# Performance work log

Hardware: AMD Instinct MI355X
Metric: run time of the kernel (lower is better)

## Reference

```python
import jax, jax.numpy as jnp
import numpy as np

B, T_SRC, T_TGT = 2048, 32, 32
D = 512            # d_model
D_SRC, D_TGT = 100, 80
L = 2              # n_layers


def setup_inputs() -> dict:
    key = jax.random.key(0)
    ks = jax.random.split(key, 16)
    s = 1.0 / float(np.sqrt(D))  # torch LSTM init scale
    u = lambda k, shape: jax.random.uniform(k, shape, jnp.float32, -s, s)
    return {
        "src": jax.random.randint(ks[0], (B, T_SRC), 0, D_SRC, dtype=jnp.int32),
        "tgt": jax.random.randint(ks[1], (B, T_TGT), 0, D_TGT, dtype=jnp.int32),
        "enc_emb": jax.random.normal(ks[2], (D_SRC, D), jnp.float32),
        "dec_emb": jax.random.normal(ks[3], (D_TGT, D), jnp.float32),
        "enc_Wih": u(ks[4], (L, 4 * D, D)),
        "enc_Whh": u(ks[5], (L, 4 * D, D)),
        "enc_bih": u(ks[6], (L, 4 * D)),
        "enc_bhh": u(ks[7], (L, 4 * D)),
        "dec_Wih": u(ks[8], (L, 4 * D, D)),
        "dec_Whh": u(ks[9], (L, 4 * D, D)),
        "dec_bih": u(ks[10], (L, 4 * D)),
        "dec_bhh": u(ks[11], (L, 4 * D)),
        "post_W": u(ks[12], (D_TGT, D)),
        "post_b": u(ks[13], (D_TGT,)),
    }


def lstm_cell(x, h, c, Wih, Whh, bih, bhh):
    # PyTorch gate order: i, f, g, o
    gates = x @ Wih.T + bih + h @ Whh.T + bhh  # [B, 4D]
    i, f, g, o = jnp.split(gates, 4, axis=-1)
    c_new = jax.nn.sigmoid(f) * c + jax.nn.sigmoid(i) * jnp.tanh(g)
    h_new = jax.nn.sigmoid(o) * jnp.tanh(c_new)
    return h_new, c_new


def reference(src, tgt, enc_emb, dec_emb, enc_Wih, enc_Whh, enc_bih, enc_bhh,
              dec_Wih, dec_Whh, dec_bih, dec_bhh, post_W, post_b):
    # Eval-mode forward: dropout = identity, teacher forcing disabled
    # (tf = random() < ratio AND self.training is False at inference).
    n_layers = enc_Wih.shape[0]
    Bb = src.shape[0]
    Dm = enc_emb.shape[1]

    # ---- encoder: multi-layer LSTM over src embeddings ----
    x = enc_emb[src].swapaxes(0, 1)  # [T_src, B, D]
    hs, cs = [], []
    z = jnp.zeros((Bb, Dm), x.dtype)
    for l in range(n_layers):
        def step(carry, xt, l=l):
            h, c = carry
            h, c = lstm_cell(xt, h, c, enc_Wih[l], enc_Whh[l], enc_bih[l], enc_bhh[l])
            return (h, c), h
        (hT, cT), x = jax.lax.scan(step, (z, z), x)
        hs.append(hT)
        cs.append(cT)
    h0 = jnp.stack(hs)  # [L, B, D]
    c0 = jnp.stack(cs)  # [L, B, D]

    prev0 = dec_emb[tgt[:, 0]]  # [B, D]

    def dec_step(carry, _):
        h, c, prev = carry
        x = prev
        new_h, new_c = [], []
        for l in range(n_layers):
            hl, cl = lstm_cell(x, h[l], c[l], dec_Wih[l], dec_Whh[l], dec_bih[l], dec_bhh[l])
            new_h.append(hl)
            new_c.append(cl)
            x = hl
        logits = x @ post_W.T + post_b          # [B, d_tgt]
        pred = jnp.argmax(logits, axis=-1)       # [B]
        prev = dec_emb[pred]                     # [B, D]
        return (jnp.stack(new_h), jnp.stack(new_c), prev), logits

    _, out = jax.lax.scan(dec_step, (h0, c0, prev0), None, length=tgt.shape[1])
    return out.swapaxes(0, 1)  # [B, T_tgt, d_tgt]
```

## Files before the change

### kernel.cpp

```cpp
#include <hip/hip_runtime.h>
#include <hip/hip_bf16.h>

#define B_  2048
#define T_  32
#define D_  512
#define G_  2048
#define VT_ 80
#define BD  (B_ * D_)
#define LWE ((size_t)G_ * D_)

typedef _Float16 half8 __attribute__((ext_vector_type(8)));
typedef _Float16 half4_t __attribute__((ext_vector_type(4)));
typedef float    f32x4 __attribute__((ext_vector_type(4)));

static __device__ __forceinline__ float sigm(float x) {
    return 1.0f / (1.0f + expf(-x));
}

typedef __attribute__((address_space(1))) unsigned int gas_u32;
typedef __attribute__((address_space(3))) unsigned int las_u32;
static __device__ __forceinline__ void glds16(const void* src, void* dst) {
    __builtin_amdgcn_global_load_lds(
        (gas_u32*)(unsigned long long)(size_t)src,
        (las_u32*)(unsigned int)(size_t)dst, 16, 0, 0);
}

#define WBX() do {                                        \
    asm volatile("s_waitcnt vmcnt(10)" ::: "memory");     \
    __builtin_amdgcn_s_barrier();                         \
    __builtin_amdgcn_sched_barrier(0);                    \
} while (0)

__global__ void zero_ws(int4* __restrict__ p, int n) {
    int i = blockIdx.x * blockDim.x + threadIdx.x;
    if (i < n) p[i] = int4{0, 0, 0, 0};
}
__global__ void init_pred(const int* __restrict__ tgt, int* __restrict__ pred) {
    int i = blockIdx.x * blockDim.x + threadIdx.x;
    if (i < B_) pred[i] = tgt[i * T_];
}

__global__ void split_weights(const float* __restrict__ s0, const float* __restrict__ s1,
                              const float* __restrict__ s2, const float* __restrict__ s3,
                              const float* __restrict__ s4, const float* __restrict__ s5,
                              _Float16* __restrict__ Wbase) {
    int g = blockIdx.x * blockDim.x + threadIdx.x;
    int mat = g >> 17;
    int rem = g & 131071;
    int np  = rem >> 6;
    int kq  = rem & 63;
    const float* src = (mat == 0) ? s0 : (mat == 1) ? s1 : (mat == 2) ? s2
                     : (mat == 3) ? s3 : (mat == 4) ? s4 : s5;
    int n = (np & 3) * D_ + (np >> 2);
    const float* sp = src + (size_t)n * D_ + kq * 8;
    float4 v0 = ((const float4*)sp)[0], v1 = ((const float4*)sp)[1];
    float x[8] = {v0.x, v0.y, v0.z, v0.w, v1.x, v1.y, v1.z, v1.w};
    _Float16 hi[8], lo[8];
    #pragma unroll
    for (int u = 0; u < 8; ++u) {
        hi[u] = (_Float16)x[u];
        lo[u] = (_Float16)(x[u] - (float)hi[u]);
    }
    int tile = (np >> 4) * 16 + (kq >> 2);
    int lane = (np & 15) | ((kq & 3) << 4);
    size_t e = (size_t)tile * 512 + (size_t)lane * 8;
    _Float16* Whi = Wbase + (size_t)mat * (2 * LWE);
    _Float16* Wlo = Whi + LWE;
    *(half8*)(Whi + e) = *(half8*)hi;
    *(half8*)(Wlo + e) = *(half8*)lo;
}

__global__ void split_postW(const float* __restrict__ pw,
                            _Float16* __restrict__ Ph, _Float16* __restrict__ Pl) {
    int g = blockIdx.x * blockDim.x + threadIdx.x;
    if (g >= VT_ * 64) return;
    int v = g >> 6, kq = g & 63;
    const float* sp = pw + (size_t)v * D_ + kq * 8;
    float4 v0 = ((const float4*)sp)[0], v1 = ((const float4*)sp)[1];
    float x[8] = {v0.x, v0.y, v0.z, v0.w, v1.x, v1.y, v1.z, v1.w};
    _Float16 hi[8], lo[8];
    #pragma unroll
    for (int u = 0; u < 8; ++u) {
        hi[u] = (_Float16)x[u];
        lo[u] = (_Float16)(x[u] - (float)hi[u]);
    }
    int tile = (v >> 4) * 16 + (kq >> 2);
    int lane = (v & 15) | ((kq & 3) << 4);
    size_t e = (size_t)tile * 512 + (size_t)lane * 8;
    *(half8*)(Ph + e) = *(half8*)hi;
    *(half8*)(Pl + e) = *(half8*)lo;
}

__global__ void perm_bias(const float* __restrict__ ebih, const float* __restrict__ ebhh,
                          const float* __restrict__ dbih, const float* __restrict__ dbhh,
                          float* __restrict__ biasP) {
    int i = blockIdx.x * blockDim.x + threadIdx.x;
    int cfg = i >> 11, np = i & 2047;
    int n = (np & 3) * D_ + (np >> 2);
    const float* bi = ((cfg < 2) ? ebih : dbih) + (cfg & 1) * G_;
    const float* bh = ((cfg < 2) ? ebhh : dbhh) + (cfg & 1) * G_;
    biasP[cfg * G_ + np] = bi[n] + bh[n];
}

__global__ __launch_bounds__(256) void compute_P(
    const float* __restrict__ enc_emb, const float* __restrict__ dec_emb,
    const float* __restrict__ encW0,   const float* __restrict__ decW0,
    float* __restrict__ P) {
    __shared__ float es[10][D_];
    __shared__ float part[4][64][10];
    int by = blockIdx.y;
    bool enc = (by < 10);
    int r0 = enc ? by * 10 : 100 + (by - 10) * 10;
    int s0 = enc ? by * 10 : (by - 10) * 10;
    const float* emb = enc ? enc_emb : dec_emb;
    const float* W   = enc ? encW0 : decW0;
    int tid = threadIdx.x;
    #pragma unroll
    for (int it = 0; it < 5; ++it) {
        int i4 = it * 256 + tid;
        int rr = i4 >> 7, cc = i4 & 127;
        ((float4*)es[rr])[cc] = ((const float4*)(emb + (size_t)(s0 + rr) * D_))[cc];
    }
    __syncthreads();
    int o   = tid & 63;
    int seg = tid >> 6;
    int np = blockIdx.x * 64 + o;
    int n = (np & 3) * D_ + (np >> 2);
    const float* wr = W + (size_t)n * D_ + seg * 128;
    float acc[10];
    #pragma unroll
    for (int rr = 0; rr < 10; ++rr) acc[rr] = 0.f;
    for (int k = 0; k < 128; k += 4) {
        float4 w4 = *(const float4*)(wr + k);
        int kb = seg * 128 + k;
        #pragma unroll
        for (int rr = 0; rr < 10; ++rr)
            acc[rr] += es[rr][kb] * w4.x + es[rr][kb+1] * w4.y
                     + es[rr][kb+2] * w4.z + es[rr][kb+3] * w4.w;
    }
    #pragma unroll
    for (int rr = 0; rr < 10; ++rr) part[seg][o][rr] = acc[rr];
    __syncthreads();
    for (int i = tid; i < 640; i += 256) {
        int o2 = i & 63, rr = i >> 6;
        P[(size_t)(r0 + rr) * G_ + blockIdx.x * 64 + o2] =
            (part[0][o2][rr] + part[1][o2][rr]) + (part[2][o2][rr] + part[3][o2][rr]);
    }
}

struct CellJob {
    const _Float16 *a0h, *a0l, *w0h, *w0l;
    int kclo0, kchi0;
    const _Float16 *a1h, *a1l, *w1h, *w1l;
    int kclo1, kchi1;
    const float *biasP;
    const float *P;
    const int  *idx;
    int idx_stride, emb_rows;
    float *c_io;
    _Float16 *hh_out, *hl_out;
};

__global__ __launch_bounds__(512, 2) void lstm_cell_mfma(CellJob J0, CellJob J1) {
    const CellJob J = (blockIdx.z == 0) ? J0 : J1;
    __shared__ __align__(128) char smem[65536];
    float (*gf)[68] = (float (*)[68])smem;

    const int tid  = threadIdx.x;
    const int w    = tid >> 6;
    const int lane = tid & 63;
    const int g    = w >> 2;
    const int mw   = w & 3;
    const int id   = blockIdx.x;
    const int xcd  = id & 7;
    const int rest = id >> 3;
    const int mt   = ((rest & 3) << 1) | (xcd >> 2);
    const int bx   = ((rest >> 2) << 2) | (xcd & 3);
    const int m0   = mt * 256;

    const _Float16* Ah = g ? J.a1h : J.a0h;
    const _Float16* Al = g ? J.a1l : J.a0l;
    const _Float16* Wh = g ? J.w1h : J.w0h;
    const _Float16* Wl = g ? J.w1l : J.w0l;
    const int kclo = g ? J.kclo1 : J.kclo0;
    const int kchi = g ? J.kchi1 : J.kchi0;

    const int afr = (m0 >> 4) + mw * 4;
    const int wfr = bx * 4;

    f32x4 acc[4][4];
    #pragma unroll
    for (int i = 0; i < 4; ++i)
        #pragma unroll
        for (int j = 0; j < 4; ++j) acc[i][j] = f32x4{0.f, 0.f, 0.f, 0.f};

    char* const sb = smem + w * 2048;
    const char* const rg0 = smem + (g << 13);

    auto stage = [&](int buf, int kc) {
        size_t toff = (((size_t)(wfr + (w & 3)) * 16 + kc) << 9) + (size_t)lane * 8;
        char* d = sb + buf * 16384;
        glds16(Wh + toff, d);
        glds16(Wl + toff, d + 1024);
    };
    auto ldA = [&](half8* A8, int kc) {
        size_t lo8 = (size_t)lane * 8;
        #pragma unroll
        for (int i = 0; i < 4; ++i) {
            size_t off = (((size_t)(afr + i) * 16 + kc) << 9) + lo8;
            A8[i]     = *(const half8*)(Ah + off);
            A8[4 + i] = *(const half8*)(Al + off);
        }
    };
    auto domfma = [&](const half8* A8, int buf) {
        const char* r = rg0 + buf * 16384;
        size_t lo16 = (size_t)lane * 16;
        #pragma unroll
        for (int j = 0; j < 4; ++j) {
            half8 Bh = *(const half8*)(r + j * 2048 + lo16);
            half8 Bl = *(const half8*)(r + j * 2048 + 1024 + lo16);
            #pragma unroll
            for (int i = 0; i < 4; ++i) {
                acc[i][j] = __builtin_amdgcn_mfma_f32_16x16x32_f16(A8[i], Bh, acc[i][j], 0, 0, 0);
                acc[i][j] = __builtin_amdgcn_mfma_f32_16x16x32_f16(A8[i], Bl, acc[i][j], 0, 0, 0);
                acc[i][j] = __builtin_amdgcn_mfma_f32_16x16x32_f16(A8[4 + i], Bh, acc[i][j], 0, 0, 0);
            }
        }
    };

    half8 A0[8], A1[8];
    const int nit = (kchi - kclo) >> 2;

    ldA(A0, kclo);
    stage(0, kclo);
    stage(1, kclo + 1);
    asm volatile("s_waitcnt vmcnt(0)" ::: "memory");
    __builtin_amdgcn_s_barrier();
    __builtin_amdgcn_sched_barrier(0);

    for (int it = 0; it < nit; ++it) {
        const int k0 = kclo + (it << 2);
        ldA(A1, k0 + 1); stage(2, k0 + 2); domfma(A0, 0); WBX();
        ldA(A0, k0 + 2); stage(3, k0 + 3); domfma(A1, 1); WBX();
        ldA(A1, k0 + 3); stage(0, k0 + 4); domfma(A0, 2); WBX();
        ldA(A0, k0 + 4); stage(1, k0 + 5); domfma(A1, 3); WBX();
    }
    asm volatile("s_waitcnt vmcnt(0)" ::: "memory");
    __syncthreads();

    const int rbase = (lane >> 4) << 2;
    const int cbase = lane & 15;
    for (int p = 0; p < 2; ++p) {
        if (g == 0 && (mw >> 1) == p) {
            #pragma unroll
            for (int i = 0; i < 4; ++i) {
                int mrow = (mw & 1) * 64 + i * 16 + rbase;
                #pragma unroll
                for (int j = 0; j < 4; ++j) {
                    int nc = j * 16 + cbase;
                    #pragma unroll
                    for (int r = 0; r < 4; ++r)
                        gf[mrow + r][nc] = acc[i][j][r];
                }
            }
        }
        __syncthreads();
        if (g == 1 && (mw >> 1) == p) {
            #pragma unroll
            for (int i = 0; i < 4; ++i) {
                int mrow = (mw & 1) * 64 + i * 16 + rbase;
                #pragma unroll
                for (int j = 0; j < 4; ++j) {
                    int nc = j * 16 + cbase;
                    #pragma unroll
                    for (int r = 0; r < 4; ++r)
                        gf[mrow + r][nc] += acc[i][j][r];
                }
            }
        }
        __syncthreads();
        {
            int mr = tid >> 2, q = tid & 3;
            int mg = m0 + p * 128 + mr;
            const float4* brow = (const float4*)(J.biasP + (bx << 6));
            const float4* Pr = nullptr;
            if (J.P) {
                int s = J.idx[mg * J.idx_stride];
                s = min(max(s, 0), J.emb_rows - 1);
                Pr = (const float4*)(J.P + (size_t)s * G_ + (bx << 6));
            }
            float* crow = J.c_io + (size_t)mg * D_ + (bx << 4) + (q << 2);
            float4 cv = *(float4*)crow;
            _Float16 hh4[4], hl4[4];
            #pragma unroll
            for (int e = 0; e < 4; ++e) {
                int dl = (q << 2) + e;
                float4 g4 = *(float4*)&gf[mr][dl << 2];
                float4 b4 = brow[dl];
                float gi = g4.x + b4.x, gF = g4.y + b4.y;
                float gg = g4.z + b4.z, go = g4.w + b4.w;
                if (Pr) {
                    float4 p4 = Pr[dl];
                    gi += p4.x; gF += p4.y; gg += p4.z; go += p4.w;
                }
                float cc = (&cv.x)[e];
                float cn = sigm(gF) * cc + sigm(gi) * tanhf(gg);
                float hn = sigm(go) * tanhf(cn);
                (&cv.x)[e] = cn;
                _Float16 hH = (_Float16)hn;
                hh4[e] = hH;
                hl4[e] = (_Float16)(hn - (float)hH);
            }
            *(float4*)crow = cv;
            int kk = (bx << 4) + (q << 2);
            size_t hoff = ((size_t)((mg >> 4) * 16 + (kk >> 5)) << 9)
                        + (size_t)((mg & 15) | (((kk >> 3) & 3) << 4)) * 8
                        + ((q & 1) << 2);
            *(half4_t*)(J.hh_out + hoff) = *(half4_t*)hh4;
            *(half4_t*)(J.hl_out + hoff) = *(half4_t*)hl4;
        }
        __syncthreads();
    }
}

__global__ __launch_bounds__(64) void logits_mfma(
    const _Float16* __restrict__ Ah, const _Float16* __restrict__ Al,
    const _Float16* __restrict__ Bh, const _Float16* __restrict__ Bl,
    const float* __restrict__ postb, float* __restrict__ out,
    int t, int* __restrict__ pred) {
    __shared__ float gf2[16][85];
    __shared__ float pb[VT_];
    const int lane = threadIdx.x;
    const int m0  = blockIdx.x * 16;
    const int afr = blockIdx.x;

    f32x4 acc[5];
    #pragma unroll
    for (int j = 0; j < 5; ++j) acc[j] = f32x4{0.f, 0.f, 0.f, 0.f};

    size_t lo8 = (size_t)lane * 8;
    for (int kc = 0; kc < 16; ++kc) {
        half8 Ahh, All, Bh8[5], Bl8[5];
        {
            size_t off = (((size_t)afr * 16 + kc) << 9) + lo8;
            Ahh = *(const half8*)(Ah + off);
            All = *(const half8*)(Al + off);
        }
        #pragma unroll
        for (int j = 0; j < 5; ++j) {
            size_t off = (((size_t)(j * 16 + kc)) << 9) + lo8;
            Bh8[j] = *(const half8*)(Bh + off);
            Bl8[j] = *(const half8*)(Bl + off);
        }
        #pragma unroll
        for (int j = 0; j < 5; ++j) {
            acc[j] = __builtin_amdgcn_mfma_f32_16x16x32_f16(Ahh, Bh8[j], acc[j], 0, 0, 0);
            acc[j] = __builtin_amdgcn_mfma_f32_16x16x32_f16(Ahh, Bl8[j], acc[j], 0, 0, 0);
            acc[j] = __builtin_amdgcn_mfma_f32_16x16x32_f16(All, Bh8[j], acc[j], 0, 0, 0);
        }
    }

    if (lane < 40) ((float2*)pb)[lane] = ((const float2*)postb)[lane];
    const int quad = lane >> 4, c = lane & 15;
    #pragma unroll
    for (int j = 0; j < 5; ++j)
        #pragma unroll
        for (int r = 0; r < 4; ++r)
            gf2[quad * 4 + r][j * 16 + c] = acc[j][r];
    __syncthreads();
    if (lane < 16) {
        int r = lane;
        float best = -3.4e38f; int bi = 0;
        #pragma unroll
        for (int v = 0; v < VT_; ++v) {
            float x = gf2[r][v] + pb[v];
            if (x > best) { best = x; bi = v; }
        }
        pred[m0 + r] = bi;
        float* orow = out + (size_t)(m0 + r) * (T_ * VT_) + (size_t)t * VT_;
        #pragma unroll
        for (int v4 = 0; v4 < VT_ / 4; ++v4) {
            float4 g4 = *(float4*)&gf2[r][v4 * 4];
            float4 b4 = *(float4*)&pb[v4 * 4];
            float4 o4 = {g4.x + b4.x, g4.y + b4.y, g4.z + b4.z, g4.w + b4.w};
            *(float4*)(orow + v4 * 4) = o4;
        }
    }
}

extern "C" void kernel_launch(void* const* d_in, const int* in_sizes, int n_in,
                              void* d_out, int out_size, void* d_ws, size_t ws_size,
                              hipStream_t stream) {
    (void)in_sizes; (void)n_in; (void)out_size; (void)ws_size;

    const int*   src     = (const int*)d_in[0];
    const int*   tgt     = (const int*)d_in[1];
    const float* enc_emb = (const float*)d_in[2];
    const float* dec_emb = (const float*)d_in[3];
    const float* enc_Wih = (const float*)d_in[4];
    const float* enc_Whh = (const float*)d_in[5];
    const float* enc_bih = (const float*)d_in[6];
    const float* enc_bhh = (const float*)d_in[7];
    const float* dec_Wih = (const float*)d_in[8];
    const float* dec_Whh = (const float*)d_in[9];
    const float* dec_bih = (const float*)d_in[10];
    const float* dec_bhh = (const float*)d_in[11];
    const float* post_W  = (const float*)d_in[12];
    const float* post_b  = (const float*)d_in[13];

    char* wsb = (char*)d_ws;
    int*   pred  = (int*)wsb;
    float* biasB = (float*)(wsb + 16384);
    float* Ptab  = (float*)(wsb + 16384 + 32768);
    char*  zbase = wsb + 16384 + 32768 + 180 * G_ * 4;
    float* C0 = (float*)zbase;
    float* C1 = C0 + BD;
    _Float16* Hh00 = (_Float16*)(C1 + BD);
    _Float16* Hh10 = Hh00 + BD;
    _Float16* Hl00 = Hh10 + BD;
    _Float16* Hl10 = Hl00 + BD;
    _Float16* Hh01 = Hl10 + BD;
    _Float16* Hh11 = Hh01 + BD;
    _Float16* Hl01 = Hh11 + BD;
    _Float16* Hl11 = Hl01 + BD;
    _Float16* Wb   = Hl11 + BD;
    _Float16* PwH  = Wb + 6 * 2 * LWE;
    _Float16* PwL  = PwH + (size_t)VT_ * D_;

    _Float16* Hhi[2][2] = { { Hh00, Hh01 }, { Hh10, Hh11 } };
    _Float16* Hlo[2][2] = { { Hl00, Hl01 }, { Hl10, Hl11 } };
    float*    Cp[2]     = { C0, C1 };
    auto WP = [&](int m, int pl) { return Wb + (size_t)m * (2 * LWE) + (size_t)pl * LWE; };

    float* out = (float*)d_out;

    zero_ws<<<4096, 256, 0, stream>>>((int4*)zbase, (16 * 1024 * 1024) / 16);
    init_pred<<<8, 256, 0, stream>>>(tgt, pred);
    split_weights<<<3072, 256, 0, stream>>>(
        enc_Whh, enc_Wih + LWE, enc_Whh + LWE,
        dec_Whh, dec_Wih + LWE, dec_Whh + LWE, Wb);
    split_postW<<<20, 256, 0, stream>>>(post_W, PwH, PwL);
    perm_bias<<<32, 256, 0, stream>>>(enc_bih, enc_bhh, dec_bih, dec_bhh, biasB);
    {
        dim3 gP(32, 18);
        compute_P<<<gP, 256, 0, stream>>>(enc_emb, dec_emb, enc_Wih, dec_Wih, Ptab);
    }

    dim3 grid1(256, 1, 1);
    dim3 grid2(256, 1, 2);
    int c0 = 0, c1 = 0;

    auto mkL0 = [&](bool enc, const int* ix, int stride, int rows) {
        int m = enc ? 0 : 3;
        CellJob j;
        j.a0h = Hhi[0][c0]; j.a0l = Hlo[0][c0];
        j.w0h = WP(m, 0);   j.w0l = WP(m, 1);
        j.kclo0 = 0; j.kchi0 = 8;
        j.a1h = Hhi[0][c0]; j.a1l = Hlo[0][c0];
        j.w1h = WP(m, 0);   j.w1l = WP(m, 1);
        j.kclo1 = 8; j.kchi1 = 16;
        j.biasP = biasB + (enc ? 0 : 2) * G_;
        j.P = enc ? Ptab : Ptab + (size_t)100 * G_;
        j.idx = ix; j.idx_stride = stride; j.emb_rows = rows;
        j.c_io = Cp[0];
        j.hh_out = Hhi[0][c0 ^ 1]; j.hl_out = Hlo[0][c0 ^ 1];
        return j;
    };
    auto mkL1 = [&](bool enc) {
        int mi = enc ? 1 : 4, mh = enc ? 2 : 5;
        CellJob j;
        j.a0h = Hhi[0][c0]; j.a0l = Hlo[0][c0];
        j.w0h = WP(mi, 0);  j.w0l = WP(mi, 1);
        j.kclo0 = 0; j.kchi0 = 16;
        j.a1h = Hhi[1][c1]; j.a1l = Hlo[1][c1];
        j.w1h = WP(mh, 0);  j.w1l = WP(mh, 1);
        j.kclo1 = 0; j.kchi1 = 16;
        j.biasP = biasB + (enc ? 1 : 3) * G_;
        j.P = nullptr; j.idx = nullptr; j.idx_stride = 0; j.emb_rows = 0;
        j.c_io = Cp[1];
        j.hh_out = Hhi[1][c1 ^ 1]; j.hl_out = Hlo[1][c1 ^ 1];
        return j;
    };

    {
        CellJob j0 = mkL0(true, src + 0, T_, 100);
        lstm_cell_mfma<<<grid1, 512, 0, stream>>>(j0, j0);
        c0 ^= 1;
        for (int t = 0; t < T_ - 1; ++t) {
            CellJob jA = mkL1(true);
            CellJob jB = mkL0(true, src + t + 1, T_, 100);
            lstm_cell_mfma<<<grid2, 512, 0, stream>>>(jA, jB);
            c1 ^= 1; c0 ^= 1;
        }
        CellJob jZ = mkL1(true);
        lstm_cell_mfma<<<grid1, 512, 0, stream>>>(jZ, jZ);
        c1 ^= 1;
    }

    for (int t = 0; t < T_; ++t) {
        CellJob j0 = mkL0(false, pred, 1, VT_);
        lstm_cell_mfma<<<grid1, 512, 0, stream>>>(j0, j0);
        c0 ^= 1;
        CellJob j1 = mkL1(false);
        lstm_cell_mfma<<<grid1, 512, 0, stream>>>(j1, j1);
        c1 ^= 1;
        logits_mfma<<<128, 64, 0, stream>>>(
            Hhi[1][c1], Hlo[1][c1], PwH, PwL, post_b, out, t, pred);
    }
}
```

Baseline: 4.603 ms.

## Halve LSTM cell M-tile to 128 rows, triple-buffer weights, double grid

The LSTM cell GEMM kernel now uses a 128-row M tile instead of 256, so each wave holds 2 A fragments instead of 4 and the grid doubles to 512 blocks per job. The weight staging ring drops from four LDS buffers to three, cutting shared memory to 48KB, and the launch bound asks for higher occupancy. The epilogue becomes a single pass, and the vmcnt wait threshold is lowered to match the smaller in-flight load count. This targets more parallelism and latency hiding in the small per-timestep GEMMs. The cost is that each weight tile is reused across fewer rows, so weight traffic from L2 doubles.

```diff
diff --git a/kernel.cpp b/kernel.cpp
--- a/kernel.cpp
+++ b/kernel.cpp
@@ -26,7 +26,7 @@
 }
 
 #define WBX() do {                                        \
-    asm volatile("s_waitcnt vmcnt(10)" ::: "memory");     \
+    asm volatile("s_waitcnt vmcnt(6)" ::: "memory");      \
     __builtin_amdgcn_s_barrier();                         \
     __builtin_amdgcn_sched_barrier(0);                    \
 } while (0)
@@ -161,9 +161,9 @@
     _Float16 *hh_out, *hl_out;
 };
 
-__global__ __launch_bounds__(512, 2) void lstm_cell_mfma(CellJob J0, CellJob J1) {
+__global__ __launch_bounds__(512, 6) void lstm_cell_mfma(CellJob J0, CellJob J1) {
     const CellJob J = (blockIdx.z == 0) ? J0 : J1;
-    __shared__ __align__(128) char smem[65536];
+    __shared__ __align__(128) char smem[49152];
     float (*gf)[68] = (float (*)[68])smem;
 
     const int tid  = threadIdx.x;
@@ -172,11 +172,9 @@
     const int g    = w >> 2;
     const int mw   = w & 3;
     const int id   = blockIdx.x;
-    const int xcd  = id & 7;
-    const int rest = id >> 3;
-    const int mt   = ((rest & 3) << 1) | (xcd >> 2);
-    const int bx   = ((rest >> 2) << 2) | (xcd & 3);
-    const int m0   = mt * 256;
+    const int mt   = id & 15;
+    const int bx   = id >> 4;
+    const int m0   = mt * 128;
 
     const _Float16* Ah = g ? J.a1h : J.a0h;
     const _Float16* Al = g ? J.a1l : J.a0l;
@@ -185,12 +183,12 @@
     const int kclo = g ? J.kclo1 : J.kclo0;
     const int kchi = g ? J.kchi1 : J.kchi0;
 
-    const int afr = (m0 >> 4) + mw * 4;
+    const int afr = (m0 >> 4) + mw * 2;
     const int wfr = bx * 4;
 
-    f32x4 acc[4][4];
-    #pragma unroll
-    for (int i = 0; i < 4; ++i)
+    f32x4 acc[2][4];
+    #pragma unroll
+    for (int i = 0; i < 2; ++i)
         #pragma unroll
         for (int j = 0; j < 4; ++j) acc[i][j] = f32x4{0.f, 0.f, 0.f, 0.f};
 
@@ -206,10 +204,10 @@
     auto ldA = [&](half8* A8, int kc) {
         size_t lo8 = (size_t)lane * 8;
         #pragma unroll
-        for (int i = 0; i < 4; ++i) {
+        for (int i = 0; i < 2; ++i) {
             size_t off = (((size_t)(afr + i) * 16 + kc) << 9) + lo8;
             A8[i]     = *(const half8*)(Ah + off);
-            A8[4 + i] = *(const half8*)(Al + off);
+            A8[2 + i] = *(const half8*)(Al + off);
         }
     };
     auto domfma = [&](const half8* A8, int buf) {
@@ -220,16 +218,16 @@
             half8 Bh = *(const half8*)(r + j * 2048 + lo16);
             half8 Bl = *(const half8*)(r + j * 2048 + 1024 + lo16);
             #pragma unroll
-            for (int i = 0; i < 4; ++i) {
+            for (int i = 0; i < 2; ++i) {
                 acc[i][j] = __builtin_amdgcn_mfma_f32_16x16x32_f16(A8[i], Bh, acc[i][j], 0, 0, 0);
                 acc[i][j] = __builtin_amdgcn_mfma_f32_16x16x32_f16(A8[i], Bl, acc[i][j], 0, 0, 0);
-                acc[i][j] = __builtin_amdgcn_mfma_f32_16x16x32_f16(A8[4 + i], Bh, acc[i][j], 0, 0, 0);
+                acc[i][j] = __builtin_amdgcn_mfma_f32_16x16x32_f16(A8[2 + i], Bh, acc[i][j], 0, 0, 0);
             }
         }
     };
 
-    half8 A0[8], A1[8];
-    const int nit = (kchi - kclo) >> 2;
+    half8 A0[4], A1[4];
+    const int P = kchi - kclo;
 
     ldA(A0, kclo);
     stage(0, kclo);
@@ -238,88 +236,96 @@
     __builtin_amdgcn_s_barrier();
     __builtin_amdgcn_sched_barrier(0);
 
-    for (int it = 0; it < nit; ++it) {
-        const int k0 = kclo + (it << 2);
-        ldA(A1, k0 + 1); stage(2, k0 + 2); domfma(A0, 0); WBX();
-        ldA(A0, k0 + 2); stage(3, k0 + 3); domfma(A1, 1); WBX();
-        ldA(A1, k0 + 3); stage(0, k0 + 4); domfma(A0, 2); WBX();
-        ldA(A0, k0 + 4); stage(1, k0 + 5); domfma(A1, 3); WBX();
-    }
+#define PHASE(u, Acur, Anext)                              \
+    if (base + (u) < P) {                                  \
+        const int kc = kclo + base + (u);                  \
+        ldA(Anext, kc + 1);                                \
+        stage(((u) + 2) % 3, kc + 2);                      \
+        domfma(Acur, (u) % 3);                             \
+        WBX();                                             \
+    }
+    for (int base = 0; base < P; base += 6) {
+        PHASE(0, A0, A1)
+        PHASE(1, A1, A0)
+        PHASE(2, A0, A1)
+        PHASE(3, A1, A0)
+        PHASE(4, A0, A1)
+        PHASE(5, A1, A0)
+    }
+#undef PHASE
+
     asm volatile("s_waitcnt vmcnt(0)" ::: "memory");
     __syncthreads();
 
     const int rbase = (lane >> 4) << 2;
     const int cbase = lane & 15;
-    for (int p = 0; p < 2; ++p) {
-        if (g == 0 && (mw >> 1) == p) {
+    if (g == 0) {
+        #pragma unroll
+        for (int i = 0; i < 2; ++i) {
+            int mrow = mw * 32 + i * 16 + rbase;
             #pragma unroll
-            for (int i = 0; i < 4; ++i) {
-                int mrow = (mw & 1) * 64 + i * 16 + rbase;
+            for (int j = 0; j < 4; ++j) {
+                int nc = j * 16 + cbase;
                 #pragma unroll
-                for (int j = 0; j < 4; ++j) {
-                    int nc = j * 16 + cbase;
-                    #pragma unroll
-                    for (int r = 0; r < 4; ++r)
-                        gf[mrow + r][nc] = acc[i][j][r];
-                }
+                for (int r = 0; r < 4; ++r)
+                    gf[mrow + r][nc] = acc[i][j][r];
             }
         }
-        __syncthreads();
-        if (g == 1 && (mw >> 1) == p) {
+    }
+    __syncthreads();
+    if (g == 1) {
+        #pragma unroll
+        for (int i = 0; i < 2; ++i) {
+            int mrow = mw * 32 + i * 16 + rbase;
             #pragma unroll
-            for (int i = 0; i < 4; ++i) {
-                int mrow = (mw & 1) * 64 + i * 16 + rbase;
+            for (int j = 0; j < 4; ++j) {
+                int nc = j * 16 + cbase;
                 #pragma unroll
-                for (int j = 0; j < 4; ++j) {
-                    int nc = j * 16 + cbase;
-                    #pragma unroll
-                    for (int r = 0; r < 4; ++r)
-                        gf[mrow + r][nc] += acc[i][j][r];
-                }
+                for (int r = 0; r < 4; ++r)
+                    gf[mrow + r][nc] += acc[i][j][r];
             }
         }
-        __syncthreads();
-        {
-            int mr = tid >> 2, q = tid & 3;
-            int mg = m0 + p * 128 + mr;
-            const float4* brow = (const float4*)(J.biasP + (bx << 6));
-            const float4* Pr = nullptr;
-            if (J.P) {
-                int s = J.idx[mg * J.idx_stride];
-                s = min(max(s, 0), J.emb_rows - 1);
-                Pr = (const float4*)(J.P + (size_t)s * G_ + (bx << 6));
+    }
+    __syncthreads();
+    {
+        int mr = tid >> 2, q = tid & 3;
+        int mg = m0 + mr;
+        const float4* brow = (const float4*)(J.biasP + (bx << 6));
+        const float4* Pr = nullptr;
+        if (J.P) {
+            int s = J.idx[mg * J.idx_stride];
+            s = min(max(s, 0), J.emb_rows - 1);
+            Pr = (const float4*)(J.P + (size_t)s * G_ + (bx << 6));
+        }
+        float* crow = J.c_io + (size_t)mg * D_ + (bx << 4) + (q << 2);
+        float4 cv = *(float4*)crow;
+        _Float16 hh4[4], hl4[4];
+        #pragma unroll
+        for (int e = 0; e < 4; ++e) {
+            int dl = (q << 2) + e;
+            float4 g4 = *(float4*)&gf[mr][dl << 2];
+            float4 b4 = brow[dl];
+            float gi = g4.x + b4.x, gF = g4.y + b4.y;
+            float gg = g4.z + b4.z, go = g4.w + b4.w;
+            if (Pr) {
+                float4 p4 = Pr[dl];
+                gi += p4.x; gF += p4.y; gg += p4.z; go += p4.w;
             }
-            float* crow = J.c_io + (size_t)mg * D_ + (bx << 4) + (q << 2);
-            float4 cv = *(float4*)crow;
-            _Float16 hh4[4], hl4[4];
-            #pragma unroll
-            for (int e = 0; e < 4; ++e) {
-                int dl = (q << 2) + e;
-                float4 g4 = *(float4*)&gf[mr][dl << 2];
-                float4 b4 = brow[dl];
-                float gi = g4.x + b4.x, gF = g4.y + b4.y;
-                float gg = g4.z + b4.z, go = g4.w + b4.w;
-                if (Pr) {
-                    float4 p4 = Pr[dl];
-                    gi += p4.x; gF += p4.y; gg += p4.z; go += p4.w;
-                }
-                float cc = (&cv.x)[e];
-                float cn = sigm(gF) * cc + sigm(gi) * tanhf(gg);
-                float hn = sigm(go) * tanhf(cn);
-                (&cv.x)[e] = cn;
-                _Float16 hH = (_Float16)hn;
-                hh4[e] = hH;
-                hl4[e] = (_Float16)(hn - (float)hH);
-            }
-            *(float4*)crow = cv;
-            int kk = (bx << 4) + (q << 2);
-            size_t hoff = ((size_t)((mg >> 4) * 16 + (kk >> 5)) << 9)
-                        + (size_t)((mg & 15) | (((kk >> 3) & 3) << 4)) * 8
-                        + ((q & 1) << 2);
-            *(half4_t*)(J.hh_out + hoff) = *(half4_t*)hh4;
-            *(half4_t*)(J.hl_out + hoff) = *(half4_t*)hl4;
-        }
-        __syncthreads();
+            float cc = (&cv.x)[e];
+            float cn = sigm(gF) * cc + sigm(gi) * tanhf(gg);
+            float hn = sigm(go) * tanhf(cn);
+            (&cv.x)[e] = cn;
+            _Float16 hH = (_Float16)hn;
+            hh4[e] = hH;
+            hl4[e] = (_Float16)(hn - (float)hH);
+        }
+        *(float4*)crow = cv;
+        int kk = (bx << 4) + (q << 2);
+        size_t hoff = ((size_t)((mg >> 4) * 16 + (kk >> 5)) << 9)
+                    + (size_t)((mg & 15) | (((kk >> 3) & 3) << 4)) * 8
+                    + ((q & 1) << 2);
+        *(half4_t*)(J.hh_out + hoff) = *(half4_t*)hh4;
+        *(half4_t*)(J.hl_out + hoff) = *(half4_t*)hl4;
     }
 }
 
@@ -446,8 +452,8 @@
         compute_P<<<gP, 256, 0, stream>>>(enc_emb, dec_emb, enc_Wih, dec_Wih, Ptab);
     }
 
-    dim3 grid1(256, 1, 1);
-    dim3 grid2(256, 1, 2);
+    dim3 grid1(512, 1, 1);
+    dim3 grid2(512, 1, 2);
     int c0 = 0, c1 = 0;
 
     auto mkL0 = [&](bool enc, const int* ix, int stride, int rows) {
```

Measured after the change: 6.676 ms. 1.45x slower.

## Replace per-step cell launches with a persistent cooperative kernel keeping weights and cell state on-chip

Applied to the files above, without the earlier changes.

Swaps the roughly 130 separate cell and logits launches for one cooperative persistent kernel that uses grid.sync between timesteps. Each block loads its slice of the recurrent weights into LDS once per phase, keeps the LSTM cell state in registers, and also computes the logits and argmax itself. This targets launch overhead, repeated weight streaming and the global c read/write. In exchange it relies on grid-wide barriers and all 256 blocks being co-resident. The encoder layers split across XCD groups, the decoder layers serialize, and the A operands are re-read from global memory without double buffering.

```diff
diff --git a/kernel.cpp b/kernel.cpp
--- a/kernel.cpp
+++ b/kernel.cpp
@@ -1,5 +1,8 @@
 #include <hip/hip_runtime.h>
 #include <hip/hip_bf16.h>
+#include <hip/hip_cooperative_groups.h>
+
+namespace cg = cooperative_groups;
 
 #define B_  2048
 #define T_  32
@@ -13,6 +16,8 @@
 typedef _Float16 half4_t __attribute__((ext_vector_type(4)));
 typedef float    f32x4 __attribute__((ext_vector_type(4)));
 
+#define MFMA16(a, b, c) __builtin_amdgcn_mfma_f32_16x16x32_f16(a, b, c, 0, 0, 0)
+
 static __device__ __forceinline__ float sigm(float x) {
     return 1.0f / (1.0f + expf(-x));
 }
@@ -24,12 +29,6 @@
         (gas_u32*)(unsigned long long)(size_t)src,
         (las_u32*)(unsigned int)(size_t)dst, 16, 0, 0);
 }
-
-#define WBX() do {                                        \
-    asm volatile("s_waitcnt vmcnt(10)" ::: "memory");     \
-    __builtin_amdgcn_s_barrier();                         \
-    __builtin_amdgcn_sched_barrier(0);                    \
-} while (0)
 
 __global__ void zero_ws(int4* __restrict__ p, int n) {
     int i = blockIdx.x * blockDim.x + threadIdx.x;
@@ -148,244 +147,220 @@
     }
 }
 
-struct CellJob {
-    const _Float16 *a0h, *a0l, *w0h, *w0l;
-    int kclo0, kchi0;
-    const _Float16 *a1h, *a1l, *w1h, *w1l;
-    int kclo1, kchi1;
-    const float *biasP;
-    const float *P;
-    const int  *idx;
-    int idx_stride, emb_rows;
-    float *c_io;
-    _Float16 *hh_out, *hl_out;
+struct PersistArgs {
+    const _Float16 *W0, *W1, *W2, *W3, *W4, *W5;
+    const _Float16 *PwH, *PwL;
+    const float *biasB;
+    const float *Ptab;
+    const int *src;
+    int *pred;
+    const float *postb;
+    float *out;
+    _Float16 *Hh00, *Hl00, *Hh01, *Hl01;
+    _Float16 *Hh10, *Hl10, *Hh11, *Hl11;
 };
 
-__global__ __launch_bounds__(512, 2) void lstm_cell_mfma(CellJob J0, CellJob J1) {
-    const CellJob J = (blockIdx.z == 0) ? J0 : J1;
-    __shared__ __align__(128) char smem[65536];
-    float (*gf)[68] = (float (*)[68])smem;
-
+__global__ void __launch_bounds__(512, 1) lstm_persistent(PersistArgs A) {
+    extern __shared__ char dsm[];
+    cg::grid_group grid = cg::this_grid();
+
+    const int b    = blockIdx.x;
+    const int xcd  = b & 7;
+    const int grp  = (xcd >= 4) ? 1 : 0;
+    const int gi   = (b >> 3) * 4 + (xcd & 3);
     const int tid  = threadIdx.x;
-    const int w    = tid >> 6;
+    const int wv   = tid >> 6;
     const int lane = tid & 63;
-    const int g    = w >> 2;
-    const int mw   = w & 3;
-    const int id   = blockIdx.x;
-    const int xcd  = id & 7;
-    const int rest = id >> 3;
-    const int mt   = ((rest & 3) << 1) | (xcd >> 2);
-    const int bx   = ((rest >> 2) << 2) | (xcd & 3);
-    const int m0   = mt * 256;
-
-    const _Float16* Ah = g ? J.a1h : J.a0h;
-    const _Float16* Al = g ? J.a1l : J.a0l;
-    const _Float16* Wh = g ? J.w1h : J.w0h;
-    const _Float16* Wl = g ? J.w1l : J.w0l;
-    const int kclo = g ? J.kclo1 : J.kclo0;
-    const int kchi = g ? J.kchi1 : J.kchi0;
-
-    const int afr = (m0 >> 4) + mw * 4;
-    const int wfr = bx * 4;
-
-    f32x4 acc[4][4];
-    #pragma unroll
-    for (int i = 0; i < 4; ++i)
-        #pragma unroll
-        for (int j = 0; j < 4; ++j) acc[i][j] = f32x4{0.f, 0.f, 0.f, 0.f};
-
-    char* const sb = smem + w * 2048;
-    const char* const rg0 = smem + (g << 13);
-
-    auto stage = [&](int buf, int kc) {
-        size_t toff = (((size_t)(wfr + (w & 3)) * 16 + kc) << 9) + (size_t)lane * 8;
-        char* d = sb + buf * 16384;
-        glds16(Wh + toff, d);
-        glds16(Wl + toff, d + 1024);
-    };
-    auto ldA = [&](half8* A8, int kc) {
-        size_t lo8 = (size_t)lane * 8;
-        #pragma unroll
-        for (int i = 0; i < 4; ++i) {
-            size_t off = (((size_t)(afr + i) * 16 + kc) << 9) + lo8;
-            A8[i]     = *(const half8*)(Ah + off);
-            A8[4 + i] = *(const half8*)(Al + off);
+
+    float* scr = (float*)(dsm + 65536 + wv * 1280);
+
+    float cst[16];
+    #pragma unroll
+    for (int f = 0; f < 16; ++f) cst[f] = 0.f;
+
+    auto stageW = [&](const _Float16* Wbase, int slot) {
+        const _Float16* Whi = Wbase;
+        const _Float16* Wlo = Wbase + LWE;
+        for (int j = wv; j < 32; j += 8) {
+            int kc = j >> 1, pl = j & 1;
+            const _Float16* s = (pl ? Wlo : Whi)
+                              + (((size_t)(gi * 16 + kc)) << 9) + (size_t)lane * 8;
+            glds16(s, dsm + slot * 32768 + kc * 2048 + pl * 1024);
         }
     };
-    auto domfma = [&](const half8* A8, int buf) {
-        const char* r = rg0 + buf * 16384;
-        size_t lo16 = (size_t)lane * 16;
+
+    auto cell = [&](int nmat,
+                    const _Float16* Axh, const _Float16* Axl,
+                    const _Float16* Arh, const _Float16* Arl,
+                    int cfg, const float* Prow,
+                    const int* idx, int idxstride, int idxoff, int idxmax,
+                    _Float16* Hho, _Float16* Hlo_) {
+        f32x4 acc[16];
         #pragma unroll
-        for (int j = 0; j < 4; ++j) {
-            half8 Bh = *(const half8*)(r + j * 2048 + lo16);
-            half8 Bl = *(const half8*)(r + j * 2048 + 1024 + lo16);
+        for (int f = 0; f < 16; ++f) acc[f] = f32x4{0.f, 0.f, 0.f, 0.f};
+        const size_t lo8  = (size_t)lane * 8;
+        const size_t lo16 = (size_t)lane * 16;
+        const int mi0 = wv * 16;
+        for (int kc = 0; kc < 16; ++kc) {
+            const char* wb = dsm + kc * 2048 + lo16;
+            half8 B0h = *(const half8*)(wb);
+            half8 B0l = *(const half8*)(wb + 1024);
+            half8 B1h = {}, B1l = {};
+            if (nmat == 2) {
+                B1h = *(const half8*)(wb + 32768);
+                B1l = *(const half8*)(wb + 32768 + 1024);
+            }
             #pragma unroll
-            for (int i = 0; i < 4; ++i) {
-                acc[i][j] = __builtin_amdgcn_mfma_f32_16x16x32_f16(A8[i], Bh, acc[i][j], 0, 0, 0);
-                acc[i][j] = __builtin_amdgcn_mfma_f32_16x16x32_f16(A8[i], Bl, acc[i][j], 0, 0, 0);
-                acc[i][j] = __builtin_amdgcn_mfma_f32_16x16x32_f16(A8[4 + i], Bh, acc[i][j], 0, 0, 0);
-            }
+            for (int f = 0; f < 16; ++f) {
+                size_t off = (((size_t)((mi0 + f) * 16 + kc)) << 9) + lo8;
+                half8 axh = *(const half8*)(Axh + off);
+                half8 axl = *(const half8*)(Axl + off);
+                acc[f] = MFMA16(axh, B0h, acc[f]);
+                acc[f] = MFMA16(axh, B0l, acc[f]);
+                acc[f] = MFMA16(axl, B0h, acc[f]);
+                if (nmat == 2) {
+                    half8 arh = *(const half8*)(Arh + off);
+                    half8 arl = *(const half8*)(Arl + off);
+                    acc[f] = MFMA16(arh, B1h, acc[f]);
+                    acc[f] = MFMA16(arh, B1l, acc[f]);
+                    acc[f] = MFMA16(arl, B1h, acc[f]);
+                }
+            }
+        }
+        const int rr0  = (lane >> 4) << 2;
+        const int ccol = lane & 15;
+        const int row  = lane >> 2;
+        const int dd   = lane & 3;
+        const int d    = gi * 4 + dd;
+        const float4 bvec = *(const float4*)(A.biasB + cfg * G_ + gi * 16 + dd * 4);
+        const size_t hbase = (size_t)(row | (((d >> 3) & 3) << 4)) * 8 + (d & 7);
+        #pragma unroll
+        for (int f = 0; f < 16; ++f) {
+            scr[(rr0 + 0) * 20 + ccol] = acc[f][0];
+            scr[(rr0 + 1) * 20 + ccol] = acc[f][1];
+            scr[(rr0 + 2) * 20 + ccol] = acc[f][2];
+            scr[(rr0 + 3) * 20 + ccol] = acc[f][3];
+            asm volatile("s_waitcnt lgkmcnt(0)" ::: "memory");
+            float4 gv = *(const float4*)(scr + row * 20 + dd * 4);
+            asm volatile("s_waitcnt lgkmcnt(0)" ::: "memory");
+            float xi = gv.x + bvec.x, xf = gv.y + bvec.y;
+            float xg = gv.z + bvec.z, xo = gv.w + bvec.w;
+            if (Prow) {
+                int m = (mi0 + f) * 16 + row;
+                int s = idx[m * idxstride + idxoff];
+                s = min(max(s, 0), idxmax - 1);
+                const float4 pv = *(const float4*)(Prow + (size_t)s * G_ + gi * 16 + dd * 4);
+                xi += pv.x; xf += pv.y; xg += pv.z; xo += pv.w;
+            }
+            float cn = sigm(xf) * cst[f] + sigm(xi) * tanhf(xg);
+            float hn = sigm(xo) * tanhf(cn);
+            cst[f] = cn;
+            _Float16 hH = (_Float16)hn;
+            _Float16 hL = (_Float16)(hn - (float)hH);
+            size_t hoff = (((size_t)((mi0 + f) * 16 + (d >> 5))) << 9) + hbase;
+            Hho[hoff]  = hH;
+            Hlo_[hoff] = hL;
         }
     };
 
-    half8 A0[8], A1[8];
-    const int nit = (kchi - kclo) >> 2;
-
-    ldA(A0, kclo);
-    stage(0, kclo);
-    stage(1, kclo + 1);
-    asm volatile("s_waitcnt vmcnt(0)" ::: "memory");
-    __builtin_amdgcn_s_barrier();
-    __builtin_amdgcn_sched_barrier(0);
-
-    for (int it = 0; it < nit; ++it) {
-        const int k0 = kclo + (it << 2);
-        ldA(A1, k0 + 1); stage(2, k0 + 2); domfma(A0, 0); WBX();
-        ldA(A0, k0 + 2); stage(3, k0 + 3); domfma(A1, 1); WBX();
-        ldA(A1, k0 + 3); stage(0, k0 + 4); domfma(A0, 2); WBX();
-        ldA(A0, k0 + 4); stage(1, k0 + 5); domfma(A1, 3); WBX();
-    }
+    auto logits = [&](int t, const _Float16* H1h, const _Float16* H1l) {
+        float* scr2 = (float*)(dsm + 65536);
+        float* pb   = scr2 + 16 * 88;
+        if (tid < VT_) pb[tid] = A.postb[tid];
+        if (wv < 5) {
+            const int j = wv;
+            f32x4 acc = f32x4{0.f, 0.f, 0.f, 0.f};
+            const size_t lo8 = (size_t)lane * 8;
+            for (int kc = 0; kc < 16; ++kc) {
+                size_t aoff = (((size_t)(gi * 16 + kc)) << 9) + lo8;
+                half8 ah = *(const half8*)(H1h + aoff);
+                half8 al = *(const half8*)(H1l + aoff);
+                size_t boff = (((size_t)(j * 16 + kc)) << 9) + lo8;
+                half8 bh = *(const half8*)(A.PwH + boff);
+                half8 bl = *(const half8*)(A.PwL + boff);
+                acc = MFMA16(ah, bh, acc);
+                acc = MFMA16(ah, bl, acc);
+                acc = MFMA16(al, bh, acc);
+            }
+            const int q = lane >> 4, c = lane & 15;
+            #pragma unroll
+            for (int r = 0; r < 4; ++r)
+                scr2[(q * 4 + r) * 88 + j * 16 + c] = acc[r];
+        }
+        __syncthreads();
+        if (tid < 16) {
+            const int r = tid;
+            float best = -3.4e38f; int bi = 0;
+            #pragma unroll
+            for (int v = 0; v < VT_; ++v) {
+                float x = scr2[r * 88 + v] + pb[v];
+                if (x > best) { best = x; bi = v; }
+            }
+            A.pred[gi * 16 + r] = bi;
+            float* orow = A.out + (size_t)(gi * 16 + r) * (T_ * VT_) + (size_t)t * VT_;
+            #pragma unroll
+            for (int v4 = 0; v4 < VT_; v4 += 4) {
+                float4 g4 = *(float4*)(scr2 + r * 88 + v4);
+                float4 b4 = *(float4*)(pb + v4);
+                *(float4*)(orow + v4) = float4{g4.x + b4.x, g4.y + b4.y,
+                                               g4.z + b4.z, g4.w + b4.w};
+            }
+        }
+        __syncthreads();
+    };
+
+    if (grp == 0) stageW(A.W0, 0);
+    else { stageW(A.W1, 0); stageW(A.W2, 1); }
     asm volatile("s_waitcnt vmcnt(0)" ::: "memory");
     __syncthreads();
 
-    const int rbase = (lane >> 4) << 2;
-    const int cbase = lane & 15;
-    for (int p = 0; p < 2; ++p) {
-        if (g == 0 && (mw >> 1) == p) {
-            #pragma unroll
-            for (int i = 0; i < 4; ++i) {
-                int mrow = (mw & 1) * 64 + i * 16 + rbase;
-                #pragma unroll
-                for (int j = 0; j < 4; ++j) {
-                    int nc = j * 16 + cbase;
-                    #pragma unroll
-                    for (int r = 0; r < 4; ++r)
-                        gf[mrow + r][nc] = acc[i][j][r];
-                }
-            }
-        }
-        __syncthreads();
-        if (g == 1 && (mw >> 1) == p) {
-            #pragma unroll
-            for (int i = 0; i < 4; ++i) {
-                int mrow = (mw & 1) * 64 + i * 16 + rbase;
-                #pragma unroll
-                for (int j = 0; j < 4; ++j) {
-                    int nc = j * 16 + cbase;
-                    #pragma unroll
-                    for (int r = 0; r < 4; ++r)
-                        gf[mrow + r][nc] += acc[i][j][r];
-                }
-            }
-        }
-        __syncthreads();
-        {
-            int mr = tid >> 2, q = tid & 3;
-            int mg = m0 + p * 128 + mr;
-            const float4* brow = (const float4*)(J.biasP + (bx << 6));
-            const float4* Pr = nullptr;
-            if (J.P) {
-                int s = J.idx[mg * J.idx_stride];
-                s = min(max(s, 0), J.emb_rows - 1);
-                Pr = (const float4*)(J.P + (size_t)s * G_ + (bx << 6));
-            }
-            float* crow = J.c_io + (size_t)mg * D_ + (bx << 4) + (q << 2);
-            float4 cv = *(float4*)crow;
-            _Float16 hh4[4], hl4[4];
-            #pragma unroll
-            for (int e = 0; e < 4; ++e) {
-                int dl = (q << 2) + e;
-                float4 g4 = *(float4*)&gf[mr][dl << 2];
-                float4 b4 = brow[dl];
-                float gi = g4.x + b4.x, gF = g4.y + b4.y;
-                float gg = g4.z + b4.z, go = g4.w + b4.w;
-                if (Pr) {
-                    float4 p4 = Pr[dl];
-                    gi += p4.x; gF += p4.y; gg += p4.z; go += p4.w;
-                }
-                float cc = (&cv.x)[e];
-                float cn = sigm(gF) * cc + sigm(gi) * tanhf(gg);
-                float hn = sigm(go) * tanhf(cn);
-                (&cv.x)[e] = cn;
-                _Float16 hH = (_Float16)hn;
-                hh4[e] = hH;
-                hl4[e] = (_Float16)(hn - (float)hH);
-            }
-            *(float4*)crow = cv;
-            int kk = (bx << 4) + (q << 2);
-            size_t hoff = ((size_t)((mg >> 4) * 16 + (kk >> 5)) << 9)
-                        + (size_t)((mg & 15) | (((kk >> 3) & 3) << 4)) * 8
-                        + ((q & 1) << 2);
-            *(half4_t*)(J.hh_out + hoff) = *(half4_t*)hh4;
-            *(half4_t*)(J.hl_out + hoff) = *(half4_t*)hl4;
-        }
-        __syncthreads();
-    }
-}
-
-__global__ __launch_bounds__(64) void logits_mfma(
-    const _Float16* __restrict__ Ah, const _Float16* __restrict__ Al,
-    const _Float16* __restrict__ Bh, const _Float16* __restrict__ Bl,
-    const float* __restrict__ postb, float* __restrict__ out,
-    int t, int* __restrict__ pred) {
-    __shared__ float gf2[16][85];
-    __shared__ float pb[VT_];
-    const int lane = threadIdx.x;
-    const int m0  = blockIdx.x * 16;
-    const int afr = blockIdx.x;
-
-    f32x4 acc[5];
-    #pragma unroll
-    for (int j = 0; j < 5; ++j) acc[j] = f32x4{0.f, 0.f, 0.f, 0.f};
-
-    size_t lo8 = (size_t)lane * 8;
-    for (int kc = 0; kc < 16; ++kc) {
-        half8 Ahh, All, Bh8[5], Bl8[5];
-        {
-            size_t off = (((size_t)afr * 16 + kc) << 9) + lo8;
-            Ahh = *(const half8*)(Ah + off);
-            All = *(const half8*)(Al + off);
-        }
-        #pragma unroll
-        for (int j = 0; j < 5; ++j) {
-            size_t off = (((size_t)(j * 16 + kc)) << 9) + lo8;
-            Bh8[j] = *(const half8*)(Bh + off);
-            Bl8[j] = *(const half8*)(Bl + off);
-        }
-        #pragma unroll
-        for (int j = 0; j < 5; ++j) {
-            acc[j] = __builtin_amdgcn_mfma_f32_16x16x32_f16(Ahh, Bh8[j], acc[j], 0, 0, 0);
-            acc[j] = __builtin_amdgcn_mfma_f32_16x16x32_f16(Ahh, Bl8[j], acc[j], 0, 0, 0);
-            acc[j] = __builtin_amdgcn_mfma_f32_16x16x32_f16(All, Bh8[j], acc[j], 0, 0, 0);
-        }
-    }
-
-    if (lane < 40) ((float2*)pb)[lane] = ((const float2*)postb)[lane];
-    const int quad = lane >> 4, c = lane & 15;
-    #pragma unroll
-    for (int j = 0; j < 5; ++j)
-        #pragma unroll
-        for (int r = 0; r < 4; ++r)
-            gf2[quad * 4 + r][j * 16 + c] = acc[j][r];
+    const _Float16 *h0hr = A.Hh00, *h0lr = A.Hl00;
+    _Float16 *h0hw = A.Hh01, *h0lw = A.Hl01;
+    const _Float16 *h1hr = A.Hh10, *h1lr = A.Hl10;
+    _Float16 *h1hw = A.Hh11, *h1lw = A.Hl11;
+
+#define SWAP0() { const _Float16* t1_ = h0hr; h0hr = h0hw; h0hw = (_Float16*)t1_; \
+                  const _Float16* t2_ = h0lr; h0lr = h0lw; h0lw = (_Float16*)t2_; }
+#define SWAP1() { const _Float16* t1_ = h1hr; h1hr = h1hw; h1hw = (_Float16*)t1_; \
+                  const _Float16* t2_ = h1lr; h1lr = h1lw; h1lw = (_Float16*)t2_; }
+
+    if (grp == 0)
+        cell(1, h0hr, h0lr, nullptr, nullptr, 0, A.Ptab, A.src, T_, 0, 100, h0hw, h0lw);
+    grid.sync();
+    SWAP0();
+    for (int t = 0; t < T_ - 1; ++t) {
+        if (grp == 1)
+            cell(2, h0hr, h0lr, h1hr, h1lr, 1, nullptr, nullptr, 0, 0, 1, h1hw, h1lw);
+        else
+            cell(1, h0hr, h0lr, nullptr, nullptr, 0, A.Ptab, A.src, T_, t + 1, 100, h0hw, h0lw);
+        grid.sync();
+        SWAP0(); SWAP1();
+    }
+    if (grp == 1)
+        cell(2, h0hr, h0lr, h1hr, h1lr, 1, nullptr, nullptr, 0, 0, 1, h1hw, h1lw);
+    grid.sync();
+    SWAP1();
+
+    if (grp == 0) stageW(A.W3, 0);
+    else { stageW(A.W4, 0); stageW(A.W5, 1); }
+    asm volatile("s_waitcnt vmcnt(0)" ::: "memory");
     __syncthreads();
-    if (lane < 16) {
-        int r = lane;
-        float best = -3.4e38f; int bi = 0;
-        #pragma unroll
-        for (int v = 0; v < VT_; ++v) {
-            float x = gf2[r][v] + pb[v];
-            if (x > best) { best = x; bi = v; }
-        }
-        pred[m0 + r] = bi;
-        float* orow = out + (size_t)(m0 + r) * (T_ * VT_) + (size_t)t * VT_;
-        #pragma unroll
-        for (int v4 = 0; v4 < VT_ / 4; ++v4) {
-            float4 g4 = *(float4*)&gf2[r][v4 * 4];
-            float4 b4 = *(float4*)&pb[v4 * 4];
-            float4 o4 = {g4.x + b4.x, g4.y + b4.y, g4.z + b4.z, g4.w + b4.w};
-            *(float4*)(orow + v4 * 4) = o4;
-        }
-    }
+
+    const float* Pdec = A.Ptab + (size_t)100 * G_;
+    for (int t = 0; t < T_; ++t) {
+        if (grp == 0)
+            cell(1, h0hr, h0lr, nullptr, nullptr, 2, Pdec, A.pred, 1, 0, VT_, h0hw, h0lw);
+        grid.sync();
+        SWAP0();
+        if (grp == 1)
+            cell(2, h0hr, h0lr, h1hr, h1lr, 3, nullptr, nullptr, 0, 0, 1, h1hw, h1lw);
+        grid.sync();
+        SWAP1();
+        if (grp == 0) logits(t, h1hr, h1lr);
+        grid.sync();
+    }
+#undef SWAP0
+#undef SWAP1
 }
 
 extern "C" void kernel_launch(void* const* d_in, const int* in_sizes, int n_in,
@@ -427,11 +402,6 @@
     _Float16* PwH  = Wb + 6 * 2 * LWE;
     _Float16* PwL  = PwH + (size_t)VT_ * D_;
 
-    _Float16* Hhi[2][2] = { { Hh00, Hh01 }, { Hh10, Hh11 } };
-    _Float16* Hlo[2][2] = { { Hl00, Hl01 }, { Hl10, Hl11 } };
-    float*    Cp[2]     = { C0, C1 };
-    auto WP = [&](int m, int pl) { return Wb + (size_t)m * (2 * LWE) + (size_t)pl * LWE; };
-
     float* out = (float*)d_out;
 
     zero_ws<<<4096, 256, 0, stream>>>((int4*)zbase, (16 * 1024 * 1024) / 16);
@@ -446,65 +416,26 @@
         compute_P<<<gP, 256, 0, stream>>>(enc_emb, dec_emb, enc_Wih, dec_Wih, Ptab);
     }
 
-    dim3 grid1(256, 1, 1);
-    dim3 grid2(256, 1, 2);
-    int c0 = 0, c1 = 0;
-
-    auto mkL0 = [&](bool enc, const int* ix, int stride, int rows) {
-        int m = enc ? 0 : 3;
-        CellJob j;
-        j.a0h = Hhi[0][c0]; j.a0l = Hlo[0][c0];
-        j.w0h = WP(m, 0);   j.w0l = WP(m, 1);
-        j.kclo0 = 0; j.kchi0 = 8;
-        j.a1h = Hhi[0][c0]; j.a1l = Hlo[0][c0];
-        j.w1h = WP(m, 0);   j.w1l = WP(m, 1);
-        j.kclo1 = 8; j.kchi1 = 16;
-        j.biasP = biasB + (enc ? 0 : 2) * G_;
-        j.P = enc ? Ptab : Ptab + (size_t)100 * G_;
-        j.idx = ix; j.idx_stride = stride; j.emb_rows = rows;
-        j.c_io = Cp[0];
-        j.hh_out = Hhi[0][c0 ^ 1]; j.hl_out = Hlo[0][c0 ^ 1];
-        return j;
-    };
-    auto mkL1 = [&](bool enc) {
-        int mi = enc ? 1 : 4, mh = enc ? 2 : 5;
-        CellJob j;
-        j.a0h = Hhi[0][c0]; j.a0l = Hlo[0][c0];
-        j.w0h = WP(mi, 0);  j.w0l = WP(mi, 1);
-        j.kclo0 = 0; j.kchi0 = 16;
-        j.a1h = Hhi[1][c1]; j.a1l = Hlo[1][c1];
-        j.w1h = WP(mh, 0);  j.w1l = WP(mh, 1);
-        j.kclo1 = 0; j.kchi1 = 16;
-        j.biasP = biasB + (enc ? 1 : 3) * G_;
-        j.P = nullptr; j.idx = nullptr; j.idx_stride = 0; j.emb_rows = 0;
-        j.c_io = Cp[1];
-        j.hh_out = Hhi[1][c1 ^ 1]; j.hl_out = Hlo[1][c1 ^ 1];
-        return j;
-    };
-
-    {
-        CellJob j0 = mkL0(true, src + 0, T_, 100);
-        lstm_cell_mfma<<<grid1, 512, 0, stream>>>(j0, j0);
-        c0 ^= 1;
-        for (int t = 0; t < T_ - 1; ++t) {
-            CellJob jA = mkL1(true);
-            CellJob jB = mkL0(true, src + t + 1, T_, 100);
-            lstm_cell_mfma<<<grid2, 512, 0, stream>>>(jA, jB);
-            c1 ^= 1; c0 ^= 1;
-        }
-        CellJob jZ = mkL1(true);
-        lstm_cell_mfma<<<grid1, 512, 0, stream>>>(jZ, jZ);
-        c1 ^= 1;
-    }
-
-    for (int t = 0; t < T_; ++t) {
-        CellJob j0 = mkL0(false, pred, 1, VT_);
-        lstm_cell_mfma<<<grid1, 512, 0, stream>>>(j0, j0);
-        c0 ^= 1;
-        CellJob j1 = mkL1(false);
-        lstm_cell_mfma<<<grid1, 512, 0, stream>>>(j1, j1);
-        c1 ^= 1;
-        logits_mfma<<<128, 64, 0, stream>>>(
-            Hhi[1][c1], Hlo[1][c1], PwH, PwL, post_b, out, t, pred);
-    }
-}
+    static int s_attr = 0;
+    if (!s_attr) {
+        hipFuncSetAttribute((const void*)lstm_persistent,
+                            hipFuncAttributeMaxDynamicSharedMemorySize, 75776);
+        s_attr = 1;
+    }
+    PersistArgs pa;
+    pa.W0 = Wb + (size_t)0 * (2 * LWE);
+    pa.W1 = Wb + (size_t)1 * (2 * LWE);
+    pa.W2 = Wb + (size_t)2 * (2 * LWE);
+    pa.W3 = Wb + (size_t)3 * (2 * LWE);
+    pa.W4 = Wb + (size_t)4 * (2 * LWE);
+    pa.W5 = Wb + (size_t)5 * (2 * LWE);
+    pa.PwH = PwH; pa.PwL = PwL;
+    pa.biasB = biasB; pa.Ptab = Ptab;
+    pa.src = src; pa.pred = pred;
+    pa.postb = post_b; pa.out = out;
+    pa.Hh00 = Hh00; pa.Hl00 = Hl00; pa.Hh01 = Hh01; pa.Hl01 = Hl01;
+    pa.Hh10 = Hh10; pa.Hl10 = Hl10; pa.Hh11 = Hh11; pa.Hl11 = Hl11;
+    void* kargs[] = { (void*)&pa };
+    hipLaunchCooperativeKernel((const void*)lstm_persistent, dim3(256), dim3(512),
+                               kargs, 75776, stream);
+}
```

Result: slower. 16.15 ms (+251.0%).
